# Kernel optimization log

Hardware: AMD Instinct MI355X
Metric: run time of the kernel (lower is better)

The kernel has to match this reference:

```python
import jax, jax.numpy as jnp
import numpy as np

GAUSS_START = 0.5
GAUSS_END = 5.0
N_GAUSS = 16
N_ATOMS = 3072
N_GRAPHS = 64
K_GRID = 4096


def setup_inputs() -> dict:
    key = jax.random.key(0)
    k1, k2, k3, k4 = jax.random.split(key, 4)
    coeff = jax.random.normal(k1, (N_ATOMS, N_GAUSS), dtype=jnp.float32)
    atom_coord = jax.random.normal(k2, (N_ATOMS, 3), dtype=jnp.float32)
    grid = jax.random.normal(k3, (N_GRAPHS, K_GRID, 3), dtype=jnp.float32)
    batch = jnp.sort(jax.random.randint(k4, (N_ATOMS,), 0, N_GRAPHS, dtype=jnp.int64))
    return {"coeff": coeff, "atom_coord": atom_coord, "grid": grid, "batch": batch}


def reference(coeff, atom_coord, grid, batch):
    # Precomputed gaussian widths (buffers in the torch module)
    sigma = jnp.linspace(GAUSS_START, GAUSS_END, N_GAUSS, dtype=jnp.float32)
    sigma_r = 1.0 / (sigma * np.float32(np.sqrt(2.0 * np.pi))) ** 3  # (n_gauss,)
    sigma_2r = 1.0 / sigma ** 2  # (n_gauss,)

    # Gather per-atom grid: (N, K, 3)
    sample_vec = grid[batch] - atom_coord[:, None, :]
    r2 = jnp.sum(sample_vec ** 2, axis=-1)  # (N, K)
    # Gaussian basis on grid: (N, K, n_gauss)
    orbital = jnp.exp(-r2[..., None] * sigma_2r) * sigma_r
    # Weighted sum over gaussians: (N, K)
    density = jnp.einsum('nkg,ng->nk', orbital, coeff)
    # Scatter-add atoms back to their graph: (G, K)
    return jax.ops.segment_sum(density, batch, num_segments=N_GRAPHS)
```

## Files before the change

kernel.cpp:

```cpp
#include <hip/hip_runtime.h>
#include <cmath>

constexpr int N_GAUSS = 16;
constexpr int N_GRAPHS = 64;
constexpr int K_GRID = 4096;
constexpr int KCHUNK = 256;
constexpr int CHUNKS_PER_GRAPH = K_GRID / KCHUNK;

struct GaussParams {
    float ns2[N_GAUSS];
    float b[N_GAUSS];
};

__device__ __forceinline__ float fast_exp2(float x) {
#if defined(__has_builtin)
#if __has_builtin(__builtin_amdgcn_exp2f)
    return __builtin_amdgcn_exp2f(x);
#else
    float r; asm("v_exp_f32 %0, %1" : "=v"(r) : "v"(x)); return r;
#endif
#else
    float r; asm("v_exp_f32 %0, %1" : "=v"(r) : "v"(x)); return r;
#endif
}

__global__ __launch_bounds__(KCHUNK) void GaussianOrbital_kernel(
    const float* __restrict__ coeff,
    const float* __restrict__ atom_coord,
    const float* __restrict__ grid,
    const int* __restrict__ batch,
    float* __restrict__ out,
    GaussParams p, int n_atoms)
{
    const int graph = blockIdx.x / CHUNKS_PER_GRAPH;
    const int chunk = blockIdx.x % CHUNKS_PER_GRAPH;
    const int k = chunk * KCHUNK + (int)threadIdx.x;

    int lo, hi;
    {
        int l = 0, h = n_atoms;
        while (l < h) { int m = (l + h) >> 1; if (batch[m] < graph) l = m + 1; else h = m; }
        lo = l;
        h = n_atoms;
        while (l < h) { int m = (l + h) >> 1; if (batch[m] < graph + 1) l = m + 1; else h = m; }
        hi = l;
    }
    lo = __builtin_amdgcn_readfirstlane(lo);
    hi = __builtin_amdgcn_readfirstlane(hi);

    const int gk = graph * K_GRID + k;
    const float kx = grid[gk * 3 + 0];
    const float ky = grid[gk * 3 + 1];
    const float kz = grid[gk * 3 + 2];

    float acc0 = 0.f, acc1 = 0.f, acc2 = 0.f, acc3 = 0.f;

    #pragma unroll 2
    for (int a = lo; a < hi; ++a) {
        const float ax = atom_coord[a * 3 + 0];
        const float ay = atom_coord[a * 3 + 1];
        const float az = atom_coord[a * 3 + 2];
        const float dx = kx - ax;
        const float dy = ky - ay;
        const float dz = kz - az;
        const float r2 = fmaf(dx, dx, fmaf(dy, dy, dz * dz));
        const float* __restrict__ cf = coeff + a * N_GAUSS;
        #pragma unroll
        for (int g = 0; g < N_GAUSS; g += 4) {
            acc0 = fmaf(cf[g + 0], fast_exp2(fmaf(r2, p.ns2[g + 0], p.b[g + 0])), acc0);
            acc1 = fmaf(cf[g + 1], fast_exp2(fmaf(r2, p.ns2[g + 1], p.b[g + 1])), acc1);
            acc2 = fmaf(cf[g + 2], fast_exp2(fmaf(r2, p.ns2[g + 2], p.b[g + 2])), acc2);
            acc3 = fmaf(cf[g + 3], fast_exp2(fmaf(r2, p.ns2[g + 3], p.b[g + 3])), acc3);
        }
    }

    out[gk] = (acc0 + acc1) + (acc2 + acc3);
}

extern "C" void kernel_launch(void* const* d_in, const int* in_sizes, int n_in,
                              void* d_out, int out_size, void* d_ws, size_t ws_size,
                              hipStream_t stream)
{
    const float* coeff      = (const float*)d_in[0];
    const float* atom_coord = (const float*)d_in[1];
    const float* grid       = (const float*)d_in[2];
    const int*   batch      = (const int*)d_in[3];
    float* out = (float*)d_out;
    const int n_atoms = in_sizes[0] / N_GAUSS;

    GaussParams p;
    const double sqrt2pi = 2.50662827463100050242;
    for (int g = 0; g < N_GAUSS; ++g) {
        const double sigma = 0.5 + (5.0 - 0.5) * (double)g / (double)(N_GAUSS - 1);
        p.ns2[g] = (float)(-1.44269504088896340736 / (sigma * sigma));
        const double sr = 1.0 / (sigma * sqrt2pi * sigma * sqrt2pi * sigma * sqrt2pi);
        p.b[g] = (float)(std::log2(sr));
    }

    dim3 gridDim(N_GRAPHS * CHUNKS_PER_GRAPH);
    dim3 blockDim(KCHUNK);
    hipLaunchKernelGGL(GaussianOrbital_kernel, gridDim, blockDim, 0, stream,
                       coeff, atom_coord, grid, batch, out, p, n_atoms);
}
```

Baseline: 98.29 us.

## Split atoms across blocks with atomic accumulation and packed two-point math

The kernel now tiles over fixed groups of six atoms instead of over whole graphs. Each block finds the graph ids in its group, flushes partial sums with atomicAdd whenever the graph changes, and the output is zeroed first with a memset. Each thread also handles two grid points using 2-wide float vectors so the packed FMA instructions can be used. The aim is better load balance across the uneven atom counts per graph and more work per thread. In exchange it adds many atomics, repeated loads of grid coordinates, and an extra memset launch.

Measured after the change: 87.43 us. 11.1% less time.

```diff
diff --git a/kernel.cpp b/kernel.cpp
--- a/kernel.cpp
+++ b/kernel.cpp
@@ -5,11 +5,16 @@
 constexpr int N_GRAPHS = 64;
 constexpr int K_GRID = 4096;
 constexpr int KCHUNK = 256;
-constexpr int CHUNKS_PER_GRAPH = K_GRID / KCHUNK;
+constexpr int KPER = 2;
+constexpr int KSPAN = KCHUNK * KPER;
+constexpr int CHUNKS = K_GRID / KSPAN;
+constexpr int APB = 6;
+
+typedef float v2f __attribute__((ext_vector_type(2)));
 
 struct GaussParams {
-    float ns2[N_GAUSS];
-    float b[N_GAUSS];
+    v2f ns2[N_GAUSS / 2];
+    v2f b[N_GAUSS / 2];
 };
 
 __device__ __forceinline__ float fast_exp2(float x) {
@@ -32,49 +37,77 @@
     float* __restrict__ out,
     GaussParams p, int n_atoms)
 {
-    const int graph = blockIdx.x / CHUNKS_PER_GRAPH;
-    const int chunk = blockIdx.x % CHUNKS_PER_GRAPH;
-    const int k = chunk * KCHUNK + (int)threadIdx.x;
+    const int chunk = blockIdx.x;
+    const int ablk  = blockIdx.y;
+    const int t = (int)threadIdx.x;
+    const int k0 = chunk * KSPAN + t;
+    const int k1 = k0 + KCHUNK;
 
-    int lo, hi;
+    const int lo = ablk * APB;
+    int hi = lo + APB; if (hi > n_atoms) hi = n_atoms;
+
+    int cur_g = __builtin_amdgcn_readfirstlane(batch[lo]);
+
+    v2f kx, ky, kz;
     {
-        int l = 0, h = n_atoms;
-        while (l < h) { int m = (l + h) >> 1; if (batch[m] < graph) l = m + 1; else h = m; }
-        lo = l;
-        h = n_atoms;
-        while (l < h) { int m = (l + h) >> 1; if (batch[m] < graph + 1) l = m + 1; else h = m; }
-        hi = l;
+        const int b0 = (cur_g * K_GRID + k0) * 3;
+        const int b1 = (cur_g * K_GRID + k1) * 3;
+        kx = (v2f){grid[b0 + 0], grid[b1 + 0]};
+        ky = (v2f){grid[b0 + 1], grid[b1 + 1]};
+        kz = (v2f){grid[b0 + 2], grid[b1 + 2]};
     }
-    lo = __builtin_amdgcn_readfirstlane(lo);
-    hi = __builtin_amdgcn_readfirstlane(hi);
 
-    const int gk = graph * K_GRID + k;
-    const float kx = grid[gk * 3 + 0];
-    const float ky = grid[gk * 3 + 1];
-    const float kz = grid[gk * 3 + 2];
+    v2f acc0 = {0.f, 0.f}, acc1 = {0.f, 0.f}, acc2 = {0.f, 0.f}, acc3 = {0.f, 0.f};
 
-    float acc0 = 0.f, acc1 = 0.f, acc2 = 0.f, acc3 = 0.f;
+    for (int a = lo; a < hi; ++a) {
+        const int g = __builtin_amdgcn_readfirstlane(batch[a]);
+        if (g != cur_g) {
+            const float s0 = (acc0.x + acc1.x) + (acc2.x + acc3.x);
+            const float s1 = (acc0.y + acc1.y) + (acc2.y + acc3.y);
+            atomicAdd(&out[cur_g * K_GRID + k0], s0);
+            atomicAdd(&out[cur_g * K_GRID + k1], s1);
+            acc0 = acc1 = acc2 = acc3 = (v2f){0.f, 0.f};
+            cur_g = g;
+            const int b0 = (cur_g * K_GRID + k0) * 3;
+            const int b1 = (cur_g * K_GRID + k1) * 3;
+            kx = (v2f){grid[b0 + 0], grid[b1 + 0]};
+            ky = (v2f){grid[b0 + 1], grid[b1 + 1]};
+            kz = (v2f){grid[b0 + 2], grid[b1 + 2]};
+        }
 
-    #pragma unroll 2
-    for (int a = lo; a < hi; ++a) {
         const float ax = atom_coord[a * 3 + 0];
         const float ay = atom_coord[a * 3 + 1];
         const float az = atom_coord[a * 3 + 2];
-        const float dx = kx - ax;
-        const float dy = ky - ay;
-        const float dz = kz - az;
-        const float r2 = fmaf(dx, dx, fmaf(dy, dy, dz * dz));
+        const v2f dx = kx - (v2f){ax, ax};
+        const v2f dy = ky - (v2f){ay, ay};
+        const v2f dz = kz - (v2f){az, az};
+        const v2f r2 = __builtin_elementwise_fma(dx, dx,
+                         __builtin_elementwise_fma(dy, dy, dz * dz));
+
         const float* __restrict__ cf = coeff + a * N_GAUSS;
+
         #pragma unroll
-        for (int g = 0; g < N_GAUSS; g += 4) {
-            acc0 = fmaf(cf[g + 0], fast_exp2(fmaf(r2, p.ns2[g + 0], p.b[g + 0])), acc0);
-            acc1 = fmaf(cf[g + 1], fast_exp2(fmaf(r2, p.ns2[g + 1], p.b[g + 1])), acc1);
-            acc2 = fmaf(cf[g + 2], fast_exp2(fmaf(r2, p.ns2[g + 2], p.b[g + 2])), acc2);
-            acc3 = fmaf(cf[g + 3], fast_exp2(fmaf(r2, p.ns2[g + 3], p.b[g + 3])), acc3);
+        for (int j = 0; j < N_GAUSS / 2; ++j) {
+            const v2f n2 = p.ns2[j], bb = p.b[j];
+            const v2f argA = __builtin_elementwise_fma(r2, (v2f){n2.x, n2.x}, (v2f){bb.x, bb.x});
+            const v2f argB = __builtin_elementwise_fma(r2, (v2f){n2.y, n2.y}, (v2f){bb.y, bb.y});
+            const v2f eA = {fast_exp2(argA.x), fast_exp2(argA.y)};
+            const v2f eB = {fast_exp2(argB.x), fast_exp2(argB.y)};
+            const float cA = cf[2 * j + 0], cB = cf[2 * j + 1];
+            if (j & 2) {
+                acc2 = __builtin_elementwise_fma((v2f){cA, cA}, eA, acc2);
+                acc3 = __builtin_elementwise_fma((v2f){cB, cB}, eB, acc3);
+            } else {
+                acc0 = __builtin_elementwise_fma((v2f){cA, cA}, eA, acc0);
+                acc1 = __builtin_elementwise_fma((v2f){cB, cB}, eB, acc1);
+            }
         }
     }
 
-    out[gk] = (acc0 + acc1) + (acc2 + acc3);
+    const float s0 = (acc0.x + acc1.x) + (acc2.x + acc3.x);
+    const float s1 = (acc0.y + acc1.y) + (acc2.y + acc3.y);
+    atomicAdd(&out[cur_g * K_GRID + k0], s0);
+    atomicAdd(&out[cur_g * K_GRID + k1], s1);
 }
 
 extern "C" void kernel_launch(void* const* d_in, const int* in_sizes, int n_in,
@@ -92,12 +125,17 @@
     const double sqrt2pi = 2.50662827463100050242;
     for (int g = 0; g < N_GAUSS; ++g) {
         const double sigma = 0.5 + (5.0 - 0.5) * (double)g / (double)(N_GAUSS - 1);
-        p.ns2[g] = (float)(-1.44269504088896340736 / (sigma * sigma));
+        const float ns2 = (float)(-1.44269504088896340736 / (sigma * sigma));
         const double sr = 1.0 / (sigma * sqrt2pi * sigma * sqrt2pi * sigma * sqrt2pi);
-        p.b[g] = (float)(std::log2(sr));
+        const float bb = (float)(std::log2(sr));
+        if (g & 1) { p.ns2[g >> 1].y = ns2; p.b[g >> 1].y = bb; }
+        else       { p.ns2[g >> 1].x = ns2; p.b[g >> 1].x = bb; }
     }
 
-    dim3 gridDim(N_GRAPHS * CHUNKS_PER_GRAPH);
+    hipMemsetAsync(d_out, 0, (size_t)out_size * sizeof(float), stream);
+
+    const int n_ablk = (n_atoms + APB - 1) / APB;
+    dim3 gridDim(CHUNKS, n_ablk);
     dim3 blockDim(KCHUNK);
     hipLaunchKernelGGL(GaussianOrbital_kernel, gridDim, blockDim, 0, stream,
                        coeff, atom_coord, grid, batch, out, p, n_atoms);
```

## Replace per-point gaussian sums with per-atom radial lookup table interpolation

Applied to the files above, without the earlier changes.

Adds a pre-pass that tabulates each atom's 16-gaussian radial density on 512 uniform radius samples up to a cutoff, stored as value/slope pairs in the workspace. The main kernel then computes the radius and linearly interpolates from the table instead of evaluating 16 exponentials per atom-point pair. This removes most transcendental work but adds a second launch and gather-style table loads, and introduces interpolation and cutoff error.

After: 86.30 us. 1.14x faster.

```diff
diff --git a/kernel.cpp b/kernel.cpp
--- a/kernel.cpp
+++ b/kernel.cpp
@@ -4,8 +4,13 @@
 constexpr int N_GAUSS = 16;
 constexpr int N_GRAPHS = 64;
 constexpr int K_GRID = 4096;
+
+constexpr int NSEG = 512;
+constexpr int TSTRIDE2 = 528;
+constexpr float RMAX = 12.0f;
+
 constexpr int KCHUNK = 256;
-constexpr int CHUNKS_PER_GRAPH = K_GRID / KCHUNK;
+constexpr int CHUNKS = K_GRID / KCHUNK;
 
 struct GaussParams {
     float ns2[N_GAUSS];
@@ -13,68 +18,88 @@
 };
 
 __device__ __forceinline__ float fast_exp2(float x) {
-#if defined(__has_builtin)
-#if __has_builtin(__builtin_amdgcn_exp2f)
     return __builtin_amdgcn_exp2f(x);
-#else
-    float r; asm("v_exp_f32 %0, %1" : "=v"(r) : "v"(x)); return r;
-#endif
-#else
-    float r; asm("v_exp_f32 %0, %1" : "=v"(r) : "v"(x)); return r;
-#endif
+}
+
+__global__ __launch_bounds__(256) void build_table_kernel(
+    const float* __restrict__ coeff,
+    float2* __restrict__ table,
+    GaussParams p)
+{
+    __shared__ float fv[257];
+    const int a = blockIdx.y;
+    const int t = (int)threadIdx.x;
+    const int n = blockIdx.x * 256 + t;
+    const float* __restrict__ cf = coeff + a * N_GAUSS;
+
+    auto eval = [&](int idx) -> float {
+        const float r = (float)idx * (RMAX / (float)NSEG);
+        const float r2 = r * r;
+        float a0 = 0.f, a1 = 0.f, a2 = 0.f, a3 = 0.f;
+        #pragma unroll
+        for (int g = 0; g < N_GAUSS; g += 4) {
+            a0 = fmaf(cf[g + 0], fast_exp2(fmaf(r2, p.ns2[g + 0], p.b[g + 0])), a0);
+            a1 = fmaf(cf[g + 1], fast_exp2(fmaf(r2, p.ns2[g + 1], p.b[g + 1])), a1);
+            a2 = fmaf(cf[g + 2], fast_exp2(fmaf(r2, p.ns2[g + 2], p.b[g + 2])), a2);
+            a3 = fmaf(cf[g + 3], fast_exp2(fmaf(r2, p.ns2[g + 3], p.b[g + 3])), a3);
+        }
+        return (a0 + a1) + (a2 + a3);
+    };
+
+    fv[t] = eval(n);
+    if (t == 255) fv[256] = eval(n + 1);
+    __syncthreads();
+    const float f0 = fv[t];
+    const float f1 = fv[t + 1];
+    table[(size_t)a * TSTRIDE2 + n] = make_float2(f0, f1 - f0);
 }
 
 __global__ __launch_bounds__(KCHUNK) void GaussianOrbital_kernel(
-    const float* __restrict__ coeff,
+    const float2* __restrict__ table,
     const float* __restrict__ atom_coord,
     const float* __restrict__ grid,
     const int* __restrict__ batch,
     float* __restrict__ out,
-    GaussParams p, int n_atoms)
+    int n_atoms)
 {
-    const int graph = blockIdx.x / CHUNKS_PER_GRAPH;
-    const int chunk = blockIdx.x % CHUNKS_PER_GRAPH;
-    const int k = chunk * KCHUNK + (int)threadIdx.x;
+    const int g = blockIdx.y;
+    const int k = blockIdx.x * KCHUNK + (int)threadIdx.x;
 
     int lo, hi;
     {
         int l = 0, h = n_atoms;
-        while (l < h) { int m = (l + h) >> 1; if (batch[m] < graph) l = m + 1; else h = m; }
+        while (l < h) { int m = (l + h) >> 1; if (batch[m] < g) l = m + 1; else h = m; }
         lo = l;
         h = n_atoms;
-        while (l < h) { int m = (l + h) >> 1; if (batch[m] < graph + 1) l = m + 1; else h = m; }
+        while (l < h) { int m = (l + h) >> 1; if (batch[m] < g + 1) l = m + 1; else h = m; }
         hi = l;
     }
     lo = __builtin_amdgcn_readfirstlane(lo);
     hi = __builtin_amdgcn_readfirstlane(hi);
 
-    const int gk = graph * K_GRID + k;
+    const int gk = g * K_GRID + k;
     const float kx = grid[gk * 3 + 0];
     const float ky = grid[gk * 3 + 1];
     const float kz = grid[gk * 3 + 2];
 
-    float acc0 = 0.f, acc1 = 0.f, acc2 = 0.f, acc3 = 0.f;
+    float acc = 0.f;
 
-    #pragma unroll 2
+    #pragma unroll 4
     for (int a = lo; a < hi; ++a) {
         const float ax = atom_coord[a * 3 + 0];
         const float ay = atom_coord[a * 3 + 1];
         const float az = atom_coord[a * 3 + 2];
-        const float dx = kx - ax;
-        const float dy = ky - ay;
-        const float dz = kz - az;
+        const float dx = kx - ax, dy = ky - ay, dz = kz - az;
         const float r2 = fmaf(dx, dx, fmaf(dy, dy, dz * dz));
-        const float* __restrict__ cf = coeff + a * N_GAUSS;
-        #pragma unroll
-        for (int g = 0; g < N_GAUSS; g += 4) {
-            acc0 = fmaf(cf[g + 0], fast_exp2(fmaf(r2, p.ns2[g + 0], p.b[g + 0])), acc0);
-            acc1 = fmaf(cf[g + 1], fast_exp2(fmaf(r2, p.ns2[g + 1], p.b[g + 1])), acc1);
-            acc2 = fmaf(cf[g + 2], fast_exp2(fmaf(r2, p.ns2[g + 2], p.b[g + 2])), acc2);
-            acc3 = fmaf(cf[g + 3], fast_exp2(fmaf(r2, p.ns2[g + 3], p.b[g + 3])), acc3);
-        }
+        float tt = __builtin_amdgcn_sqrtf(r2) * ((float)NSEG / RMAX);
+        tt = fminf(tt, (float)(NSEG - 1));
+        const int i = (int)tt;
+        const float fr = tt - (float)i;
+        const float2 e = table[(size_t)a * TSTRIDE2 + i];
+        acc += fmaf(fr, e.y, e.x);
     }
 
-    out[gk] = (acc0 + acc1) + (acc2 + acc3);
+    out[gk] = acc;
 }
 
 extern "C" void kernel_launch(void* const* d_in, const int* in_sizes, int n_in,
@@ -85,7 +110,8 @@
     const float* atom_coord = (const float*)d_in[1];
     const float* grid       = (const float*)d_in[2];
     const int*   batch      = (const int*)d_in[3];
-    float* out = (float*)d_out;
+    float* out    = (float*)d_out;
+    float2* table = (float2*)d_ws;
     const int n_atoms = in_sizes[0] / N_GAUSS;
 
     GaussParams p;
@@ -97,8 +123,14 @@
         p.b[g] = (float)(std::log2(sr));
     }
 
-    dim3 gridDim(N_GRAPHS * CHUNKS_PER_GRAPH);
-    dim3 blockDim(KCHUNK);
-    hipLaunchKernelGGL(GaussianOrbital_kernel, gridDim, blockDim, 0, stream,
-                       coeff, atom_coord, grid, batch, out, p, n_atoms);
+    {
+        dim3 gDim(2, n_atoms);
+        hipLaunchKernelGGL(build_table_kernel, gDim, dim3(256), 0, stream,
+                           coeff, table, p);
+    }
+    {
+        dim3 gDim(CHUNKS, N_GRAPHS);
+        hipLaunchKernelGGL(GaussianOrbital_kernel, gDim, dim3(KCHUNK), 0, stream,
+                           table, atom_coord, grid, batch, out, n_atoms);
+    }
 }
```
